# Performance work log

Measured on AMD Instinct MI355X. Metric: run time of the kernel, lower is better.

## Reference

```python
import jax, jax.numpy as jnp
import numpy as np

N_NODES = 100000
N_EDGES = 640000
IN_CH = 128
OUT_CH = 128


def setup_inputs() -> dict:
    key = jax.random.key(0)
    k1, k2, k3, k4, k5, k6 = jax.random.split(key, 6)
    row = jax.random.randint(k1, (N_EDGES,), 0, N_NODES, dtype=jnp.int64 if jax.config.jax_enable_x64 else jnp.int32)
    col = jax.random.randint(k2, (N_EDGES,), 0, N_NODES, dtype=jnp.int64 if jax.config.jax_enable_x64 else jnp.int32)
    vals = jax.random.uniform(k3, (N_EDGES,), dtype=jnp.float32)
    X = jax.random.normal(k4, (N_NODES, IN_CH), dtype=jnp.float32)
    weights = jax.random.normal(k5, (IN_CH, OUT_CH), dtype=jnp.float32)
    bias = jax.random.normal(k6, (OUT_CH,), dtype=jnp.float32)
    return {"row": row, "col": col, "vals": vals, "X": X, "weights": weights, "bias": bias}


def reference(row, col, vals, X, weights, bias):
    # A is sparse COO: A[row[e], col[e]] = vals[e]
    N = X.shape[0]
    # dense feature transform: [N, out]
    XTheta = X @ weights
    # D = (row_sum(A) + 1)^(-1/2)
    deg = jax.ops.segment_sum(vals, row, num_segments=N)
    D = jax.lax.rsqrt(deg + 1.0)
    # Xprime = D * (A @ (D * XTheta))
    Y = D[:, None] * XTheta                                    # [N, out]
    msgs = vals[:, None] * Y[col]                              # [E, out] gather
    AY = jax.ops.segment_sum(msgs, row, num_segments=N)        # [N, out] scatter-add
    return D[:, None] * AY + bias
```

## Files before the change

kernel.cpp:

```cpp
#include <hip/hip_runtime.h>
#include <hip/hip_bf16.h>


#define N_CH 128
#define WT_LD 136
#define FIXS 16777216.0f

typedef __attribute__((ext_vector_type(8))) short short8;
typedef __attribute__((ext_vector_type(4))) float f32x4;
typedef __attribute__((ext_vector_type(4))) unsigned short ushort4v;

__device__ inline unsigned short f2bf(float f) {
    unsigned u = __float_as_uint(f);
    return (unsigned short)((u + 0x7FFFu + ((u >> 16) & 1u)) >> 16);
}
__device__ inline float bf2f(unsigned short h) {
    return __uint_as_float(((unsigned)h) << 16);
}

__global__ __launch_bounds__(256) void rank_kernel(const int* __restrict__ row,
                                                   const float* __restrict__ vals,
                                                   unsigned long long* __restrict__ packed,
                                                   int* __restrict__ rank,
                                                   const float* __restrict__ W,
                                                   unsigned short* __restrict__ Wt,
                                                   int E, int rankBlocks) {
    if ((int)blockIdx.x >= rankBlocks) {
        int i = (blockIdx.x - rankBlocks) * 256 + threadIdx.x;
        int k = i >> 7, n = i & 127;
        Wt[n * N_CH + k] = f2bf(W[k * N_CH + n]);
        return;
    }
    int e0 = blockIdx.x * 512 + threadIdx.x;
#pragma unroll
    for (int j = 0; j < 2; ++j) {
        int e = e0 + j * 256;
        if (e < E) {
            int r = row[e];
            unsigned fx = (unsigned)(vals[e] * FIXS);
            unsigned long long old =
                atomicAdd(&packed[r], (1ULL << 32) | (unsigned long long)fx);
            rank[e] = (int)(old >> 32);
        }
    }
}

__global__ __launch_bounds__(256) void scan1_kernel(const unsigned long long* __restrict__ packed,
                                                    int* __restrict__ pos,
                                                    int* __restrict__ bsum, int N) {
    __shared__ int s[256];
    int t = threadIdx.x;
    int i = blockIdx.x * 256 + t;
    int v = (i < N) ? (int)(packed[i] >> 32) : 0;
    s[t] = v;
    __syncthreads();
    for (int off = 1; off < 256; off <<= 1) {
        int x = (t >= off) ? s[t - off] : 0;
        __syncthreads();
        s[t] += x;
        __syncthreads();
    }
    if (i < N) pos[i] = s[t] - v;
    if (t == 255) bsum[blockIdx.x] = s[t];
}

__global__ __launch_bounds__(256) void scan3_kernel(int* __restrict__ pos,
                                                    const int* __restrict__ bsum,
                                                    const unsigned long long* __restrict__ packed,
                                                    float* __restrict__ dinv, int N) {
    __shared__ int s[256];
    int t = threadIdx.x;
    int b = blockIdx.x;
    int acc = 0;
    for (int j = t; j < b; j += 256) acc += bsum[j];
    s[t] = acc;
    __syncthreads();
    for (int off = 128; off > 0; off >>= 1) {
        if (t < off) s[t] += s[t + off];
        __syncthreads();
    }
    int i = b * 256 + t;
    if (i < N) {
        pos[i] += s[0];
        float deg = (float)(unsigned)(packed[i] & 0xFFFFFFFFull) * (1.0f / FIXS);
        dinv[i] = rsqrtf(deg + 1.0f);
    }
}

__global__ __launch_bounds__(256) void gemm_place_kernel(
        const float* __restrict__ X, const unsigned short* __restrict__ Wt,
        const float* __restrict__ dinv, unsigned short* __restrict__ Ybf, int N,
        const int* __restrict__ row, const int* __restrict__ col,
        const float* __restrict__ vals, const int* __restrict__ pos,
        const int* __restrict__ rank, uint2* __restrict__ epack, int E,
        int gemmBlocks) {
    __shared__ unsigned short Wl[N_CH * WT_LD];

    if ((int)blockIdx.x >= gemmBlocks) {
        int e0 = (blockIdx.x - gemmBlocks) * 1024 + threadIdx.x;
#pragma unroll
        for (int j = 0; j < 4; ++j) {
            int e = e0 + j * 256;
            if (e < E) {
                int r = row[e];
                int p = pos[r] + rank[e];
                epack[p] = make_uint2((unsigned)col[e], __float_as_uint(vals[e]));
            }
        }
        return;
    }

    const int t = threadIdx.x;
    const short8* Wg = (const short8*)Wt;
#pragma unroll
    for (int j = 0; j < 8; ++j) {
        int idx = t + 256 * j;
        int r = idx >> 4, cc = idx & 15;
        *(short8*)(Wl + r * WT_LD + cc * 8) = Wg[idx];
    }
    __syncthreads();

    const int lane = t & 63;
    const int wv = t >> 6;
    const int m = lane & 15;
    const int q = lane >> 4;

    const int tiles = (N + 15) / 16;
    const int totalWaves = gemmBlocks * 4;
    int tile = blockIdx.x * 4 + wv;
    if (tile >= tiles) return;

    f32x4 pl[4], ph[4];
    {
        int rr = tile * 16 + m;
        if (rr >= N) rr = N - 1;
        const float* xr = X + (size_t)rr * N_CH + q * 8;
#pragma unroll
        for (int c = 0; c < 4; ++c) {
            pl[c] = *(const f32x4*)(xr + c * 32);
            ph[c] = *(const f32x4*)(xr + c * 32 + 4);
        }
    }

    while (true) {
        const int next = tile + totalWaves;
        const bool hasNext = next < tiles;

        f32x4 ql[4], qh[4];
        if (hasNext) {
            int rr2 = next * 16 + m;
            if (rr2 >= N) rr2 = N - 1;
            const float* xr2 = X + (size_t)rr2 * N_CH + q * 8;
#pragma unroll
            for (int c = 0; c < 4; ++c) {
                ql[c] = *(const f32x4*)(xr2 + c * 32);
                qh[c] = *(const f32x4*)(xr2 + c * 32 + 4);
            }
        }

        short8 a[4];
#pragma unroll
        for (int c = 0; c < 4; ++c) {
            short8 v;
            v[0] = (short)f2bf(pl[c][0]); v[1] = (short)f2bf(pl[c][1]);
            v[2] = (short)f2bf(pl[c][2]); v[3] = (short)f2bf(pl[c][3]);
            v[4] = (short)f2bf(ph[c][0]); v[5] = (short)f2bf(ph[c][1]);
            v[6] = (short)f2bf(ph[c][2]); v[7] = (short)f2bf(ph[c][3]);
            a[c] = v;
        }

        f32x4 acc[8];
#pragma unroll
        for (int tt = 0; tt < 8; ++tt) acc[tt] = (f32x4){0.f, 0.f, 0.f, 0.f};

#pragma unroll
        for (int tt = 0; tt < 8; ++tt) {
            const unsigned short* wrow = Wl + (tt * 16 + m) * WT_LD + q * 8;
#pragma unroll
            for (int c = 0; c < 4; ++c) {
                short8 b = *(const short8*)(wrow + c * 32);
                acc[tt] = __builtin_amdgcn_mfma_f32_16x16x32_bf16(b, a[c], acc[tt], 0, 0, 0);
            }
        }

        const int rr = tile * 16 + m;
        if (rr < N) {
            const float d = dinv[rr];
            unsigned short* yrow = Ybf + (size_t)rr * N_CH;
#pragma unroll
            for (int tt = 0; tt < 8; ++tt) {
                unsigned lo = (unsigned)f2bf(acc[tt][0] * d) |
                              ((unsigned)f2bf(acc[tt][1] * d) << 16);
                unsigned hi = (unsigned)f2bf(acc[tt][2] * d) |
                              ((unsigned)f2bf(acc[tt][3] * d) << 16);
                *(uint2*)(yrow + tt * 16 + q * 4) = make_uint2(lo, hi);
            }
        }

        if (!hasNext) break;
#pragma unroll
        for (int c = 0; c < 4; ++c) { pl[c] = ql[c]; ph[c] = qh[c]; }
        tile = next;
    }
}

__global__ __launch_bounds__(256) void gather_kernel(const int* __restrict__ pos,
                                                     const uint2* __restrict__ epack,
                                                     const unsigned short* __restrict__ Ybf,
                                                     const float* __restrict__ dinv,
                                                     const float* __restrict__ bias,
                                                     float* __restrict__ out, int N, int E) {
    unsigned gid = blockIdx.x * 256u + threadIdx.x;
    int n = gid >> 5;
    if (n >= N) return;
    int lane = gid & 31;
    int c = lane * 4;

    int e = pos[n];
    int end = (n + 1 < N) ? pos[n + 1] : E;

    float4 acc = make_float4(0.f, 0.f, 0.f, 0.f);
    for (; e + 4 <= end; e += 4) {
        uint2 p0 = epack[e + 0];
        uint2 p1 = epack[e + 1];
        uint2 p2 = epack[e + 2];
        uint2 p3 = epack[e + 3];
        ushort4v y0 = *(const ushort4v*)(Ybf + (size_t)p0.x * N_CH + c);
        ushort4v y1 = *(const ushort4v*)(Ybf + (size_t)p1.x * N_CH + c);
        ushort4v y2 = *(const ushort4v*)(Ybf + (size_t)p2.x * N_CH + c);
        ushort4v y3 = *(const ushort4v*)(Ybf + (size_t)p3.x * N_CH + c);
        float v0 = __uint_as_float(p0.y);
        float v1 = __uint_as_float(p1.y);
        float v2 = __uint_as_float(p2.y);
        float v3 = __uint_as_float(p3.y);
        acc.x += v0 * bf2f(y0[0]) + v1 * bf2f(y1[0]) + v2 * bf2f(y2[0]) + v3 * bf2f(y3[0]);
        acc.y += v0 * bf2f(y0[1]) + v1 * bf2f(y1[1]) + v2 * bf2f(y2[1]) + v3 * bf2f(y3[1]);
        acc.z += v0 * bf2f(y0[2]) + v1 * bf2f(y1[2]) + v2 * bf2f(y2[2]) + v3 * bf2f(y3[2]);
        acc.w += v0 * bf2f(y0[3]) + v1 * bf2f(y1[3]) + v2 * bf2f(y2[3]) + v3 * bf2f(y3[3]);
    }
    for (; e < end; ++e) {
        uint2 p = epack[e];
        float v = __uint_as_float(p.y);
        ushort4v y = *(const ushort4v*)(Ybf + (size_t)p.x * N_CH + c);
        acc.x += v * bf2f(y[0]);
        acc.y += v * bf2f(y[1]);
        acc.z += v * bf2f(y[2]);
        acc.w += v * bf2f(y[3]);
    }

    float d = dinv[n];
    float4 b = ((const float4*)bias)[lane];
    float4 o;
    o.x = acc.x * d + b.x;
    o.y = acc.y * d + b.y;
    o.z = acc.z * d + b.z;
    o.w = acc.w * d + b.w;
    ((float4*)(out + (size_t)n * N_CH))[lane] = o;
}

extern "C" void kernel_launch(void* const* d_in, const int* in_sizes, int n_in,
                              void* d_out, int out_size, void* d_ws, size_t ws_size,
                              hipStream_t stream) {
    const int*   row  = (const int*)d_in[0];
    const int*   col  = (const int*)d_in[1];
    const float* vals = (const float*)d_in[2];
    const float* X    = (const float*)d_in[3];
    const float* W    = (const float*)d_in[4];
    const float* bias = (const float*)d_in[5];
    float* out = (float*)d_out;

    const int E = in_sizes[0];
    const int N = in_sizes[3] / N_CH;
    const int nb = (N + 255) / 256;

    uint2*              epack  = (uint2*)d_ws;
    unsigned short*     Ybf    = (unsigned short*)(epack + E);
    float*              dinv   = (float*)(Ybf + (size_t)N * N_CH);
    unsigned long long* packed = (unsigned long long*)(dinv + N);
    int*                pos    = (int*)(packed + N);
    int*                rank   = pos + N;
    int*                bsum   = rank + E;
    unsigned short*     Wt     = (unsigned short*)(bsum + nb);

    hipMemsetAsync(packed, 0, (size_t)N * sizeof(unsigned long long), stream);

    const int rankBlocks = (E + 511) / 512;
    rank_kernel<<<rankBlocks + 64, 256, 0, stream>>>(row, vals, packed, rank, W, Wt,
                                                     E, rankBlocks);
    scan1_kernel<<<nb, 256, 0, stream>>>(packed, pos, bsum, N);
    scan3_kernel<<<nb, 256, 0, stream>>>(pos, bsum, packed, dinv, N);

    const int gemmBlocks = 512;
    int placeBlocks = (E + 1023) / 1024;
    gemm_place_kernel<<<gemmBlocks + placeBlocks, 256, 0, stream>>>(
        X, Wt, dinv, Ybf, N, row, col, vals, pos, rank, epack, E, gemmBlocks);

    unsigned gth = (unsigned)N * 32u;
    gather_kernel<<<(gth + 255) / 256, 256, 0, stream>>>(pos, epack, Ybf, dinv, bias, out, N, E);
}
```

Before: 202.8 us.

## Fuse all GCN stages into one cooperative persistent kernel with grid syncs

Replaces the memset plus five separate kernel launches with a single cooperative kernel. It runs the zeroing, degree/rank atomics, the two-level scan, edge placement plus bf16 MFMA GEMM, and the CSR gather as phases separated by grid.sync. The goal is to remove launch gaps and the inter-kernel drain and refill. In exchange the grid is capped at occupancy-limited persistent blocks, each phase has less parallel slack, and the scan second pass becomes a serial per-block loop over bsum. The old multi-kernel path is kept as a fallback if the cooperative launch fails.

Result: slower. 453.7 us (+123.8%).

```diff
diff --git a/kernel.cpp b/kernel.cpp
--- a/kernel.cpp
+++ b/kernel.cpp
@@ -1,5 +1,8 @@
 #include <hip/hip_runtime.h>
 #include <hip/hip_bf16.h>
+#include <hip/hip_cooperative_groups.h>
+
+namespace cg = cooperative_groups;
 
 
 #define N_CH 128
@@ -16,6 +19,227 @@
 }
 __device__ inline float bf2f(unsigned short h) {
     return __uint_as_float(((unsigned)h) << 16);
+}
+
+__global__ __launch_bounds__(256) void fused_kernel(
+        const int* __restrict__ row, const int* __restrict__ col,
+        const float* __restrict__ vals, const float* __restrict__ X,
+        const float* __restrict__ W, const float* __restrict__ bias,
+        float* __restrict__ out,
+        uint2* __restrict__ epack, unsigned short* __restrict__ Ybf,
+        float* __restrict__ dinv, unsigned long long* __restrict__ packed,
+        int* __restrict__ pos, int* __restrict__ rank,
+        int* __restrict__ bsum, unsigned short* __restrict__ Wt,
+        int N, int E, int nb) {
+    cg::grid_group grid = cg::this_grid();
+    __shared__ unsigned short Wl[N_CH * WT_LD];
+
+    const int t = threadIdx.x;
+    const int G = gridDim.x;
+    const int gtid = blockIdx.x * 256 + t;
+    const int gthreads = G * 256;
+
+    for (int i = gtid; i < N; i += gthreads) packed[i] = 0ULL;
+    for (int i = gtid; i < N_CH * N_CH; i += gthreads) {
+        int k = i >> 7, n = i & 127;
+        Wt[n * N_CH + k] = f2bf(W[k * N_CH + n]);
+    }
+    grid.sync();
+
+    for (int e = gtid; e < E; e += gthreads) {
+        int r = row[e];
+        unsigned fx = (unsigned)(vals[e] * FIXS);
+        unsigned long long old =
+            atomicAdd(&packed[r], (1ULL << 32) | (unsigned long long)fx);
+        rank[e] = (int)(old >> 32);
+    }
+    grid.sync();
+
+    int* s = (int*)Wl;
+    for (int seg = blockIdx.x; seg < nb; seg += G) {
+        int i = seg * 256 + t;
+        int v = (i < N) ? (int)(packed[i] >> 32) : 0;
+        s[t] = v;
+        __syncthreads();
+        for (int off = 1; off < 256; off <<= 1) {
+            int x = (t >= off) ? s[t - off] : 0;
+            __syncthreads();
+            s[t] += x;
+            __syncthreads();
+        }
+        if (i < N) pos[i] = s[t] - v;
+        if (t == 255) bsum[seg] = s[t];
+        __syncthreads();
+    }
+    grid.sync();
+
+    for (int seg = blockIdx.x; seg < nb; seg += G) {
+        int acc = 0;
+        for (int j = t; j < seg; j += 256) acc += bsum[j];
+        s[t] = acc;
+        __syncthreads();
+        for (int off = 128; off > 0; off >>= 1) {
+            if (t < off) s[t] += s[t + off];
+            __syncthreads();
+        }
+        int tot = s[0];
+        __syncthreads();
+        int i = seg * 256 + t;
+        if (i < N) {
+            pos[i] += tot;
+            float deg = (float)(unsigned)(packed[i] & 0xFFFFFFFFull) * (1.0f / FIXS);
+            dinv[i] = rsqrtf(deg + 1.0f);
+        }
+        __syncthreads();
+    }
+    grid.sync();
+
+    for (int e = gtid; e < E; e += gthreads) {
+        int r = row[e];
+        epack[pos[r] + rank[e]] = make_uint2((unsigned)col[e], __float_as_uint(vals[e]));
+    }
+
+    {
+        const short8* Wg = (const short8*)Wt;
+#pragma unroll
+        for (int j = 0; j < 8; ++j) {
+            int idx = t + 256 * j;
+            int r = idx >> 4, cc = idx & 15;
+            *(short8*)(Wl + r * WT_LD + cc * 8) = Wg[idx];
+        }
+        __syncthreads();
+
+        const int lane = t & 63;
+        const int wv = t >> 6;
+        const int m = lane & 15;
+        const int q = lane >> 4;
+
+        const int tiles = (N + 15) / 16;
+        const int totalWaves = G * 4;
+        int tile = blockIdx.x * 4 + wv;
+        if (tile < tiles) {
+            f32x4 pl[4], ph[4];
+            {
+                int rr = tile * 16 + m;
+                if (rr >= N) rr = N - 1;
+                const float* xr = X + (size_t)rr * N_CH + q * 8;
+#pragma unroll
+                for (int c = 0; c < 4; ++c) {
+                    pl[c] = *(const f32x4*)(xr + c * 32);
+                    ph[c] = *(const f32x4*)(xr + c * 32 + 4);
+                }
+            }
+            while (true) {
+                const int next = tile + totalWaves;
+                const bool hasNext = next < tiles;
+
+                f32x4 ql[4], qh[4];
+                if (hasNext) {
+                    int rr2 = next * 16 + m;
+                    if (rr2 >= N) rr2 = N - 1;
+                    const float* xr2 = X + (size_t)rr2 * N_CH + q * 8;
+#pragma unroll
+                    for (int c = 0; c < 4; ++c) {
+                        ql[c] = *(const f32x4*)(xr2 + c * 32);
+                        qh[c] = *(const f32x4*)(xr2 + c * 32 + 4);
+                    }
+                }
+
+                short8 a[4];
+#pragma unroll
+                for (int c = 0; c < 4; ++c) {
+                    short8 v;
+                    v[0] = (short)f2bf(pl[c][0]); v[1] = (short)f2bf(pl[c][1]);
+                    v[2] = (short)f2bf(pl[c][2]); v[3] = (short)f2bf(pl[c][3]);
+                    v[4] = (short)f2bf(ph[c][0]); v[5] = (short)f2bf(ph[c][1]);
+                    v[6] = (short)f2bf(ph[c][2]); v[7] = (short)f2bf(ph[c][3]);
+                    a[c] = v;
+                }
+
+                f32x4 acc[8];
+#pragma unroll
+                for (int tt = 0; tt < 8; ++tt) acc[tt] = (f32x4){0.f, 0.f, 0.f, 0.f};
+
+#pragma unroll
+                for (int tt = 0; tt < 8; ++tt) {
+                    const unsigned short* wrow = Wl + (tt * 16 + m) * WT_LD + q * 8;
+#pragma unroll
+                    for (int c = 0; c < 4; ++c) {
+                        short8 b = *(const short8*)(wrow + c * 32);
+                        acc[tt] = __builtin_amdgcn_mfma_f32_16x16x32_bf16(b, a[c], acc[tt], 0, 0, 0);
+                    }
+                }
+
+                const int rr = tile * 16 + m;
+                if (rr < N) {
+                    const float d = dinv[rr];
+                    unsigned short* yrow = Ybf + (size_t)rr * N_CH;
+#pragma unroll
+                    for (int tt = 0; tt < 8; ++tt) {
+                        unsigned lo = (unsigned)f2bf(acc[tt][0] * d) |
+                                      ((unsigned)f2bf(acc[tt][1] * d) << 16);
+                        unsigned hi = (unsigned)f2bf(acc[tt][2] * d) |
+                                      ((unsigned)f2bf(acc[tt][3] * d) << 16);
+                        *(uint2*)(yrow + tt * 16 + q * 4) = make_uint2(lo, hi);
+                    }
+                }
+
+                if (!hasNext) break;
+#pragma unroll
+                for (int c = 0; c < 4; ++c) { pl[c] = ql[c]; ph[c] = qh[c]; }
+                tile = next;
+            }
+        }
+    }
+    grid.sync();
+
+    {
+        const int lane = t & 31;
+        const int c = lane * 4;
+        const int ngroups = G * 8;
+        for (int n = blockIdx.x * 8 + (t >> 5); n < N; n += ngroups) {
+            int e = pos[n];
+            int end = (n + 1 < N) ? pos[n + 1] : E;
+
+            float4 acc = make_float4(0.f, 0.f, 0.f, 0.f);
+            for (; e + 4 <= end; e += 4) {
+                uint2 p0 = epack[e + 0];
+                uint2 p1 = epack[e + 1];
+                uint2 p2 = epack[e + 2];
+                uint2 p3 = epack[e + 3];
+                ushort4v y0 = *(const ushort4v*)(Ybf + (size_t)p0.x * N_CH + c);
+                ushort4v y1 = *(const ushort4v*)(Ybf + (size_t)p1.x * N_CH + c);
+                ushort4v y2 = *(const ushort4v*)(Ybf + (size_t)p2.x * N_CH + c);
+                ushort4v y3 = *(const ushort4v*)(Ybf + (size_t)p3.x * N_CH + c);
+                float v0 = __uint_as_float(p0.y);
+                float v1 = __uint_as_float(p1.y);
+                float v2 = __uint_as_float(p2.y);
+                float v3 = __uint_as_float(p3.y);
+                acc.x += v0 * bf2f(y0[0]) + v1 * bf2f(y1[0]) + v2 * bf2f(y2[0]) + v3 * bf2f(y3[0]);
+                acc.y += v0 * bf2f(y0[1]) + v1 * bf2f(y1[1]) + v2 * bf2f(y2[1]) + v3 * bf2f(y3[1]);
+                acc.z += v0 * bf2f(y0[2]) + v1 * bf2f(y1[2]) + v2 * bf2f(y2[2]) + v3 * bf2f(y3[2]);
+                acc.w += v0 * bf2f(y0[3]) + v1 * bf2f(y1[3]) + v2 * bf2f(y2[3]) + v3 * bf2f(y3[3]);
+            }
+            for (; e < end; ++e) {
+                uint2 p = epack[e];
+                float v = __uint_as_float(p.y);
+                ushort4v y = *(const ushort4v*)(Ybf + (size_t)p.x * N_CH + c);
+                acc.x += v * bf2f(y[0]);
+                acc.y += v * bf2f(y[1]);
+                acc.z += v * bf2f(y[2]);
+                acc.w += v * bf2f(y[3]);
+            }
+
+            float d = dinv[n];
+            float4 b = ((const float4*)bias)[lane];
+            float4 o;
+            o.x = acc.x * d + b.x;
+            o.y = acc.y * d + b.y;
+            o.z = acc.z * d + b.z;
+            o.w = acc.w * d + b.w;
+            ((float4*)(out + (size_t)n * N_CH))[lane] = o;
+        }
+    }
 }
 
 __global__ __launch_bounds__(256) void rank_kernel(const int* __restrict__ row,
@@ -282,19 +506,42 @@
     int*                bsum   = rank + E;
     unsigned short*     Wt     = (unsigned short*)(bsum + nb);
 
-    hipMemsetAsync(packed, 0, (size_t)N * sizeof(unsigned long long), stream);
-
-    const int rankBlocks = (E + 511) / 512;
-    rank_kernel<<<rankBlocks + 64, 256, 0, stream>>>(row, vals, packed, rank, W, Wt,
-                                                     E, rankBlocks);
-    scan1_kernel<<<nb, 256, 0, stream>>>(packed, pos, bsum, N);
-    scan3_kernel<<<nb, 256, 0, stream>>>(pos, bsum, packed, dinv, N);
-
-    const int gemmBlocks = 512;
-    int placeBlocks = (E + 1023) / 1024;
-    gemm_place_kernel<<<gemmBlocks + placeBlocks, 256, 0, stream>>>(
-        X, Wt, dinv, Ybf, N, row, col, vals, pos, rank, epack, E, gemmBlocks);
-
-    unsigned gth = (unsigned)N * 32u;
-    gather_kernel<<<(gth + 255) / 256, 256, 0, stream>>>(pos, epack, Ybf, dinv, bias, out, N, E);
-}
+    static int g_blocks = -1;
+    if (g_blocks < 0) {
+        int dev = 0;
+        hipGetDevice(&dev);
+        hipDeviceProp_t prop;
+        hipGetDeviceProperties(&prop, dev);
+        int maxB = 0;
+        hipOccupancyMaxActiveBlocksPerMultiprocessor(&maxB, (const void*)fused_kernel,
+                                                     256, 0);
+        if (maxB < 1) maxB = 1;
+        g_blocks = maxB * prop.multiProcessorCount;
+        if (g_blocks > 2048) g_blocks = 2048;
+    }
+
+    int Nv = N, Ev = E, nbv = nb;
+    void* args[] = {(void*)&row, (void*)&col, (void*)&vals, (void*)&X, (void*)&W,
+                    (void*)&bias, (void*)&out, (void*)&epack, (void*)&Ybf,
+                    (void*)&dinv, (void*)&packed, (void*)&pos, (void*)&rank,
+                    (void*)&bsum, (void*)&Wt, (void*)&Nv, (void*)&Ev, (void*)&nbv};
+
+    hipError_t err = hipLaunchCooperativeKernel((const void*)fused_kernel,
+                                                dim3(g_blocks), dim3(256),
+                                                args, 0, stream);
+    if (err != hipSuccess) {
+        hipMemsetAsync(packed, 0, (size_t)N * sizeof(unsigned long long), stream);
+        const int rankBlocks = (E + 511) / 512;
+        rank_kernel<<<rankBlocks + 64, 256, 0, stream>>>(row, vals, packed, rank, W, Wt,
+                                                         E, rankBlocks);
+        scan1_kernel<<<nb, 256, 0, stream>>>(packed, pos, bsum, N);
+        scan3_kernel<<<nb, 256, 0, stream>>>(pos, bsum, packed, dinv, N);
+        const int gemmBlocks = 512;
+        int placeBlocks = (E + 1023) / 1024;
+        gemm_place_kernel<<<gemmBlocks + placeBlocks, 256, 0, stream>>>(
+            X, Wt, dinv, Ybf, N, row, col, vals, pos, rank, epack, E, gemmBlocks);
+        unsigned gth = (unsigned)N * 32u;
+        gather_kernel<<<(gth + 255) / 256, 256, 0, stream>>>(pos, epack, Ybf, dinv,
+                                                             bias, out, N, E);
+    }
+}
```
